# Optimization experiments

Hardware: AMD Instinct MI355X
Metric: run time of the kernel (lower is better)

The kernel has to match this reference:

```python
import jax, jax.numpy as jnp
import numpy as np

LEAKY_SLOPE = 0.2  # PyG GATConv default negative_slope
EPS = 1e-16


def _gat_layer(h_in, src, dst, W, a_src, a_dst, b, concat):
    # h_in: [N, Fin]; src/dst: [Etot] (self-loops included); W: [Fin, H*C]
    N = h_in.shape[0]
    H, C = a_src.shape
    h = (h_in @ W).reshape(N, H, C)                       # [N,H,C]
    al_s = jnp.sum(h * a_src, axis=-1)                    # [N,H]
    al_d = jnp.sum(h * a_dst, axis=-1)                    # [N,H]
    e = jax.nn.leaky_relu(al_s[src] + al_d[dst], LEAKY_SLOPE)  # [E,H]
    emax = jax.ops.segment_max(e, dst, num_segments=N)    # segment softmax over dst
    p = jnp.exp(e - emax[dst])
    denom = jax.ops.segment_sum(p, dst, num_segments=N)
    alpha = p / (denom[dst] + EPS)                        # [E,H]
    out = jax.ops.segment_sum(h[src] * alpha[:, :, None], dst, num_segments=N)  # [N,H,C]
    out = out.reshape(N, H * C) if concat else out.mean(axis=1)
    return out + b


def setup_inputs() -> dict:
    key = jax.random.key(0)
    ks = jax.random.split(key, 16)
    N, E, Fin, Hd, Hh = 10000, 320000, 256, 128, 4

    def glorot(k, shape, fan_in):
        return jax.random.normal(k, shape, dtype=jnp.float32) * (1.0 / np.sqrt(fan_in))

    inp = {
        "x": jax.random.normal(ks[0], (N, Fin), dtype=jnp.float32),
        "edge_index": jax.random.randint(ks[1], (2, E), 0, N, dtype=jnp.int32),
        # conv1: Fin -> Hd x Hh heads, concat
        "W1": glorot(ks[2], (Fin, Hh * Hd), Fin),
        "a1_src": glorot(ks[3], (Hh, Hd), Hd),
        "a1_dst": glorot(ks[4], (Hh, Hd), Hd),
        "b1": jnp.zeros((Hh * Hd,), jnp.float32),
        # conv2: Hh*Hd -> Hd x Hh heads, concat
        "W2": glorot(ks[5], (Hh * Hd, Hh * Hd), Hh * Hd),
        "a2_src": glorot(ks[6], (Hh, Hd), Hd),
        "a2_dst": glorot(ks[7], (Hh, Hd), Hd),
        "b2": jnp.zeros((Hh * Hd,), jnp.float32),
        # conv3: Hh*Hd -> Hd, 1 head, concat=False (mean)
        "W3": glorot(ks[8], (Hh * Hd, Hd), Hh * Hd),
        "a3_src": glorot(ks[9], (1, Hd), Hd),
        "a3_dst": glorot(ks[10], (1, Hd), Hd),
        "b3": jnp.zeros((Hd,), jnp.float32),
        # classifier: Hd -> Hd//2 -> 2
        "Wc1": glorot(ks[11], (Hd, Hd // 2), Hd),
        "bc1": jnp.zeros((Hd // 2,), jnp.float32),
        "Wc2": glorot(ks[12], (Hd // 2, 2), Hd // 2),
        "bc2": jnp.zeros((2,), jnp.float32),
    }
    return inp


def reference(x, edge_index, W1, a1_src, a1_dst, b1, W2, a2_src, a2_dst, b2,
              W3, a3_src, a3_dst, b3, Wc1, bc1, Wc2, bc2):
    N = x.shape[0]
    loops = jnp.arange(N, dtype=edge_index.dtype)
    src = jnp.concatenate([edge_index[0], loops])  # PyG adds self-loops
    dst = jnp.concatenate([edge_index[1], loops])

    h = jax.nn.elu(_gat_layer(x, src, dst, W1, a1_src, a1_dst, b1, concat=True))
    h = jax.nn.elu(_gat_layer(h, src, dst, W2, a2_src, a2_dst, b2, concat=True))
    embeddings = _gat_layer(h, src, dst, W3, a3_src, a3_dst, b3, concat=False)  # [N, 128]
    out = jax.nn.relu(embeddings @ Wc1 + bc1) @ Wc2 + bc2  # [N, 2]
    return out, embeddings
```

## Files before the change

kernel.cpp:

```cpp
#include <hip/hip_runtime.h>
#include <cstddef>

#define LEAKY 0.2f
#define EPS_DEN 1e-16f

typedef short bf8_t __attribute__((ext_vector_type(8)));
typedef float f4_t __attribute__((ext_vector_type(4)));
typedef unsigned short us4_t __attribute__((ext_vector_type(4)));

__device__ __forceinline__ unsigned short f2bf(float f) {
    unsigned u = __float_as_uint(f);
    unsigned r = (u + 0x7fffu + ((u >> 16) & 1u)) >> 16;
    return (unsigned short)r;
}
__device__ __forceinline__ float bf2f(unsigned short h) {
    return __uint_as_float(((unsigned)h) << 16);
}

__global__ void hist_kernel(const int* __restrict__ dst, int* __restrict__ counts, int E) {
    int i = blockIdx.x * blockDim.x + threadIdx.x;
    if (i < E) atomicAdd(&counts[dst[i]], 1);
}

__global__ void scan1_kernel(int* __restrict__ cnt, int* __restrict__ bsum, int N) {
    __shared__ int s[256];
    int t = threadIdx.x;
    int i = blockIdx.x * 256 + t;
    int v = (i < N) ? cnt[i] : 0;
    s[t] = v;
    __syncthreads();
#pragma unroll
    for (int st = 1; st < 256; st <<= 1) {
        int add = (t >= st) ? s[t - st] : 0;
        __syncthreads();
        s[t] += add;
        __syncthreads();
    }
    if (i < N) cnt[i] = s[t] - v;
    if (t == 255) bsum[blockIdx.x] = s[255];
}

__global__ void scan3b_kernel(int* __restrict__ cnt, const int* __restrict__ bsum,
                              int* __restrict__ offs, int N, int NB) {
    __shared__ int sPre[64];
    __shared__ int sTot;
    int t = threadIdx.x;
    if (t < 64) {
        int v = (t < NB) ? bsum[t] : 0;
        int inc = v;
#pragma unroll
        for (int off = 1; off < 64; off <<= 1) {
            int u = __shfl_up(inc, off);
            if (t >= off) inc += u;
        }
        sPre[t] = inc - v;
        if (t == 63) sTot = inc;
    }
    __syncthreads();
    int i = blockIdx.x * 256 + t;
    if (i < N) {
        int o = cnt[i] + sPre[blockIdx.x];
        offs[i] = o;
        cnt[i] = o;
    }
    if (blockIdx.x == 0 && t == 0) offs[N] = sTot;
}

__global__ void scatter_kernel(const int* __restrict__ src, const int* __restrict__ dst,
                               int* __restrict__ cursor, int* __restrict__ csrc, int E) {
    int i = blockIdx.x * blockDim.x + threadIdx.x;
    if (i < E) {
        int d = dst[i];
        int pos = atomicAdd(&cursor[d], 1);
        csrc[pos] = src[i];
    }
}

__global__ void split_all_kernel(
    const float* __restrict__ x, unsigned short* __restrict__ xh, unsigned short* __restrict__ xl,
    int NBX,
    const float* __restrict__ W1, unsigned short* __restrict__ w1h, unsigned short* __restrict__ w1l,
    const float* __restrict__ W2, unsigned short* __restrict__ w2h, unsigned short* __restrict__ w2l,
    const float* __restrict__ W3, unsigned short* __restrict__ w3h, unsigned short* __restrict__ w3l) {
    int b = blockIdx.x, t = threadIdx.x;
    float v;
    unsigned short* ph;
    unsigned short* pl;
    int idx;
    if (b < NBX) {
        idx = b * 256 + t;
        v = x[idx];
        ph = xh; pl = xl;
    } else if (b < NBX + 512) {
        idx = (b - NBX) * 256 + t;
        int n = idx >> 8, k = idx & 255;
        v = W1[(size_t)k * 512 + n];
        ph = w1h; pl = w1l;
    } else if (b < NBX + 512 + 1024) {
        idx = (b - NBX - 512) * 256 + t;
        int n = idx >> 9, k = idx & 511;
        v = W2[(size_t)k * 512 + n];
        ph = w2h; pl = w2l;
    } else {
        idx = (b - NBX - 1536) * 256 + t;
        int n = idx >> 9, k = idx & 511;
        v = W3[(size_t)k * 128 + n];
        ph = w3h; pl = w3l;
    }
    unsigned short hv = f2bf(v);
    ph[idx] = hv;
    pl[idx] = f2bf(v - bf2f(hv));
}

__global__ __launch_bounds__(256) void mfma_gemm128_kernel(
    const unsigned short* __restrict__ Ahi, const unsigned short* __restrict__ Alo,
    const unsigned short* __restrict__ BThi, const unsigned short* __restrict__ BTlo,
    const float* __restrict__ a_src, const float* __restrict__ a_dst,
    float* __restrict__ C, float* __restrict__ als, float* __restrict__ ald,
    int M, int N, int K) {
    constexpr int BK = 32;
    __shared__ __align__(16) unsigned short sAh[128 * BK];
    __shared__ __align__(16) unsigned short sAl[128 * BK];
    __shared__ __align__(16) unsigned short sBh[128 * BK];
    __shared__ __align__(16) unsigned short sBl[128 * BK];
    __shared__ float sAls[128][2];
    __shared__ float sAld[128][2];
    int t = threadIdx.x;
    int w = t >> 6, lane = t & 63;
    int quad = lane >> 4, low = lane & 15;
    int m0 = blockIdx.y * 128, n0 = blockIdx.x * 128;
    int wm = (w & 1) * 64, wn = (w >> 1) * 64;

    f4_t acc[4][4];
#pragma unroll
    for (int i = 0; i < 4; i++)
#pragma unroll
        for (int j = 0; j < 4; j++) acc[i][j] = (f4_t){0.f, 0.f, 0.f, 0.f};

    int srow = lane >> 2;
    int schunk = lane & 3;

    for (int k0 = 0; k0 < K; k0 += BK) {
        __syncthreads();
#pragma unroll
        for (int inst = 0; inst < 2; inst++) {
            int r = w * 32 + inst * 16 + srow;
            int gm = m0 + r;
            if (gm >= M) gm = M - 1;
            size_t goff = (size_t)gm * K + k0 + schunk * 8;
            size_t loff = (size_t)(w * 2048 + inst * 1024);
            __builtin_amdgcn_global_load_lds(
                (const __attribute__((address_space(1))) void*)(Ahi + goff),
                (__attribute__((address_space(3))) void*)((char*)sAh + loff), 16, 0, 0);
            __builtin_amdgcn_global_load_lds(
                (const __attribute__((address_space(1))) void*)(Alo + goff),
                (__attribute__((address_space(3))) void*)((char*)sAl + loff), 16, 0, 0);
        }
#pragma unroll
        for (int inst = 0; inst < 2; inst++) {
            int r = w * 32 + inst * 16 + srow;
            int gn = n0 + r;
            size_t goff = (size_t)gn * K + k0 + schunk * 8;
            size_t loff = (size_t)(w * 2048 + inst * 1024);
            __builtin_amdgcn_global_load_lds(
                (const __attribute__((address_space(1))) void*)(BThi + goff),
                (__attribute__((address_space(3))) void*)((char*)sBh + loff), 16, 0, 0);
            __builtin_amdgcn_global_load_lds(
                (const __attribute__((address_space(1))) void*)(BTlo + goff),
                (__attribute__((address_space(3))) void*)((char*)sBl + loff), 16, 0, 0);
        }
        __syncthreads();

        bf8_t afh[4], bfh[4], xx[4];
#pragma unroll
        for (int i = 0; i < 4; i++) {
            int row = wm + i * 16 + low;
            afh[i] = *(const bf8_t*)&sAh[row * BK + quad * 8];
        }
#pragma unroll
        for (int j = 0; j < 4; j++) {
            int row = wn + j * 16 + low;
            bfh[j] = *(const bf8_t*)&sBh[row * BK + quad * 8];
        }
#pragma unroll
        for (int i = 0; i < 4; i++)
#pragma unroll
            for (int j = 0; j < 4; j++)
                acc[i][j] = __builtin_amdgcn_mfma_f32_16x16x32_bf16(afh[i], bfh[j], acc[i][j], 0, 0, 0);
#pragma unroll
        for (int j = 0; j < 4; j++) {
            int row = wn + j * 16 + low;
            xx[j] = *(const bf8_t*)&sBl[row * BK + quad * 8];
        }
#pragma unroll
        for (int i = 0; i < 4; i++)
#pragma unroll
            for (int j = 0; j < 4; j++)
                acc[i][j] = __builtin_amdgcn_mfma_f32_16x16x32_bf16(afh[i], xx[j], acc[i][j], 0, 0, 0);
#pragma unroll
        for (int i = 0; i < 4; i++) {
            int row = wm + i * 16 + low;
            xx[i] = *(const bf8_t*)&sAl[row * BK + quad * 8];
        }
#pragma unroll
        for (int i = 0; i < 4; i++)
#pragma unroll
            for (int j = 0; j < 4; j++)
                acc[i][j] = __builtin_amdgcn_mfma_f32_16x16x32_bf16(xx[i], bfh[j], acc[i][j], 0, 0, 0);
    }

#pragma unroll
    for (int i = 0; i < 4; i++) {
#pragma unroll
        for (int r = 0; r < 4; r++) {
            int gm = m0 + wm + i * 16 + quad * 4 + r;
            if (gm >= M) continue;
#pragma unroll
            for (int j = 0; j < 4; j++) {
                int gn = n0 + wn + j * 16 + low;
                C[(size_t)gm * N + gn] = acc[i][j][r];
            }
        }
    }

    int hd = n0 >> 7;
    float as_[4], ad_[4];
#pragma unroll
    for (int j = 0; j < 4; j++) {
        int c = wn + j * 16 + low;
        as_[j] = a_src[hd * 128 + c];
        ad_[j] = a_dst[hd * 128 + c];
    }
    int chh = wn >> 6;
#pragma unroll
    for (int i = 0; i < 4; i++) {
#pragma unroll
        for (int r = 0; r < 4; r++) {
            float v = acc[i][0][r] * as_[0] + acc[i][1][r] * as_[1] +
                      acc[i][2][r] * as_[2] + acc[i][3][r] * as_[3];
            float vd = acc[i][0][r] * ad_[0] + acc[i][1][r] * ad_[1] +
                       acc[i][2][r] * ad_[2] + acc[i][3][r] * ad_[3];
#pragma unroll
            for (int off = 1; off < 16; off <<= 1) {
                v += __shfl_xor(v, off);
                vd += __shfl_xor(vd, off);
            }
            if (low == 0) {
                int row = wm + i * 16 + quad * 4 + r;
                sAls[row][chh] = v;
                sAld[row][chh] = vd;
            }
        }
    }
    __syncthreads();
    if (t < 128) {
        int gm = m0 + t;
        if (gm < M) {
            als[gm * 4 + hd] = sAls[t][0] + sAls[t][1];
            ald[gm * 4 + hd] = sAld[t][0] + sAld[t][1];
        }
    }
}

__global__ __launch_bounds__(256) void mfma_gemm64_kernel(
    const unsigned short* __restrict__ Ahi, const unsigned short* __restrict__ Alo,
    const unsigned short* __restrict__ BThi, const unsigned short* __restrict__ BTlo,
    const float* __restrict__ a_src, const float* __restrict__ a_dst,
    float* __restrict__ C, float* __restrict__ als, float* __restrict__ ald,
    int M, int N, int K) {
    constexpr int BK = 32;
    __shared__ __align__(16) unsigned short sAh[64 * BK];
    __shared__ __align__(16) unsigned short sAl[64 * BK];
    __shared__ __align__(16) unsigned short sBh[128 * BK];
    __shared__ __align__(16) unsigned short sBl[128 * BK];
    __shared__ float sAls[64][2];
    __shared__ float sAld[64][2];
    int t = threadIdx.x;
    int w = t >> 6, lane = t & 63;
    int quad = lane >> 4, low = lane & 15;
    int m0 = blockIdx.y * 64, n0 = blockIdx.x * 128;
    int wm = (w & 1) * 32, wn = (w >> 1) * 64;

    f4_t acc[2][4];
#pragma unroll
    for (int i = 0; i < 2; i++)
#pragma unroll
        for (int j = 0; j < 4; j++) acc[i][j] = (f4_t){0.f, 0.f, 0.f, 0.f};

    int srow = lane >> 2;
    int schunk = lane & 3;

    for (int k0 = 0; k0 < K; k0 += BK) {
        __syncthreads();
        {
            int gm = m0 + w * 16 + srow;
            if (gm >= M) gm = M - 1;
            size_t goff = (size_t)gm * K + k0 + schunk * 8;
            size_t loff = (size_t)(w * 1024);
            __builtin_amdgcn_global_load_lds(
                (const __attribute__((address_space(1))) void*)(Ahi + goff),
                (__attribute__((address_space(3))) void*)((char*)sAh + loff), 16, 0, 0);
            __builtin_amdgcn_global_load_lds(
                (const __attribute__((address_space(1))) void*)(Alo + goff),
                (__attribute__((address_space(3))) void*)((char*)sAl + loff), 16, 0, 0);
        }
#pragma unroll
        for (int inst = 0; inst < 2; inst++) {
            int gn = n0 + w * 32 + inst * 16 + srow;
            size_t goff = (size_t)gn * K + k0 + schunk * 8;
            size_t loff = (size_t)(w * 2048 + inst * 1024);
            __builtin_amdgcn_global_load_lds(
                (const __attribute__((address_space(1))) void*)(BThi + goff),
                (__attribute__((address_space(3))) void*)((char*)sBh + loff), 16, 0, 0);
            __builtin_amdgcn_global_load_lds(
                (const __attribute__((address_space(1))) void*)(BTlo + goff),
                (__attribute__((address_space(3))) void*)((char*)sBl + loff), 16, 0, 0);
        }
        __syncthreads();

        bf8_t afh[2], bfh[4], xx[4];
#pragma unroll
        for (int i = 0; i < 2; i++) {
            int row = wm + i * 16 + low;
            afh[i] = *(const bf8_t*)&sAh[row * BK + quad * 8];
        }
#pragma unroll
        for (int j = 0; j < 4; j++) {
            int row = wn + j * 16 + low;
            bfh[j] = *(const bf8_t*)&sBh[row * BK + quad * 8];
        }
#pragma unroll
        for (int i = 0; i < 2; i++)
#pragma unroll
            for (int j = 0; j < 4; j++)
                acc[i][j] = __builtin_amdgcn_mfma_f32_16x16x32_bf16(afh[i], bfh[j], acc[i][j], 0, 0, 0);
#pragma unroll
        for (int j = 0; j < 4; j++) {
            int row = wn + j * 16 + low;
            xx[j] = *(const bf8_t*)&sBl[row * BK + quad * 8];
        }
#pragma unroll
        for (int i = 0; i < 2; i++)
#pragma unroll
            for (int j = 0; j < 4; j++)
                acc[i][j] = __builtin_amdgcn_mfma_f32_16x16x32_bf16(afh[i], xx[j], acc[i][j], 0, 0, 0);
#pragma unroll
        for (int i = 0; i < 2; i++) {
            int row = wm + i * 16 + low;
            xx[i] = *(const bf8_t*)&sAl[row * BK + quad * 8];
        }
#pragma unroll
        for (int i = 0; i < 2; i++)
#pragma unroll
            for (int j = 0; j < 4; j++)
                acc[i][j] = __builtin_amdgcn_mfma_f32_16x16x32_bf16(xx[i], bfh[j], acc[i][j], 0, 0, 0);
    }

#pragma unroll
    for (int i = 0; i < 2; i++) {
#pragma unroll
        for (int r = 0; r < 4; r++) {
            int gm = m0 + wm + i * 16 + quad * 4 + r;
            if (gm >= M) continue;
#pragma unroll
            for (int j = 0; j < 4; j++) {
                int gn = n0 + wn + j * 16 + low;
                C[(size_t)gm * N + gn] = acc[i][j][r];
            }
        }
    }

    float as_[4], ad_[4];
#pragma unroll
    for (int j = 0; j < 4; j++) {
        int c = wn + j * 16 + low;
        as_[j] = a_src[c];
        ad_[j] = a_dst[c];
    }
    int chh = wn >> 6;
#pragma unroll
    for (int i = 0; i < 2; i++) {
#pragma unroll
        for (int r = 0; r < 4; r++) {
            float v = acc[i][0][r] * as_[0] + acc[i][1][r] * as_[1] +
                      acc[i][2][r] * as_[2] + acc[i][3][r] * as_[3];
            float vd = acc[i][0][r] * ad_[0] + acc[i][1][r] * ad_[1] +
                       acc[i][2][r] * ad_[2] + acc[i][3][r] * ad_[3];
#pragma unroll
            for (int off = 1; off < 16; off <<= 1) {
                v += __shfl_xor(v, off);
                vd += __shfl_xor(vd, off);
            }
            if (low == 0) {
                int row = wm + i * 16 + quad * 4 + r;
                sAls[row][chh] = v;
                sAld[row][chh] = vd;
            }
        }
    }
    __syncthreads();
    if (t < 64) {
        int gm = m0 + t;
        if (gm < M) {
            als[gm] = sAls[t][0] + sAls[t][1];
            ald[gm] = sAld[t][0] + sAld[t][1];
        }
    }
}

__global__ void stats_h4_kernel(const int* __restrict__ csrc, const int* __restrict__ offs,
                                const float* __restrict__ als, const float* __restrict__ ald,
                                float* __restrict__ pbuf, float* __restrict__ psf,
                                float* __restrict__ rden, int N, int E) {
    int wave = threadIdx.x >> 6, lane = threadIdx.x & 63;
    int n = blockIdx.x * 4 + wave;
    if (n >= N) return;
    int hd = lane & 3, es = lane >> 2;
    float aldn = ald[n * 4 + hd];
    float selfe = als[n * 4 + hd] + aldn;
    selfe = selfe > 0.f ? selfe : LEAKY * selfe;
    int beg = offs[n], end = offs[n + 1];
    int deg = end - beg;
    float* pb = pbuf + (size_t)hd * E;
    float m = selfe;
    float d = 0.f;
    if (deg <= 64) {
        float eR[4];
        int nch = (deg + 15) >> 4;
        for (int k = 0; k < nch; k++) {
            int idx = beg + k * 16 + es;
            float e = -1e30f;
            if (idx < end) {
                int s = csrc[idx];
                e = als[s * 4 + hd] + aldn;
                e = e > 0.f ? e : LEAKY * e;
                m = fmaxf(m, e);
            }
            eR[k] = e;
        }
#pragma unroll
        for (int off = 4; off < 64; off <<= 1) m = fmaxf(m, __shfl_xor(m, off));
        for (int k = 0; k < nch; k++) {
            int idx = beg + k * 16 + es;
            if (idx < end) {
                float p = __expf(eR[k] - m);
                pb[idx] = p;
                d += p;
            }
        }
    } else {
        for (int base = beg; base + es < end; base += 16) {
            int idx = base + es;
            int s = csrc[idx];
            float e = als[s * 4 + hd] + aldn;
            e = e > 0.f ? e : LEAKY * e;
            pb[idx] = e;
            m = fmaxf(m, e);
        }
#pragma unroll
        for (int off = 4; off < 64; off <<= 1) m = fmaxf(m, __shfl_xor(m, off));
        for (int base = beg; base + es < end; base += 16) {
            int idx = base + es;
            float p = __expf(pb[idx] - m);
            pb[idx] = p;
            d += p;
        }
    }
#pragma unroll
    for (int off = 4; off < 64; off <<= 1) d += __shfl_xor(d, off);
    float pself = __expf(selfe - m);
    float r = 1.0f / (d + pself + EPS_DEN);
    if (es == 0) {
        psf[n * 4 + hd] = pself;
        rden[n * 4 + hd] = r;
    }
}

template <bool DO_ELU>
__global__ __launch_bounds__(64) void gat_agg_hh_kernel(
    const float* __restrict__ h, const float* __restrict__ pbuf,
    const float* __restrict__ psf, const float* __restrict__ rden,
    const int* __restrict__ csrc, const int* __restrict__ offs,
    const float* __restrict__ bias, unsigned short* __restrict__ ohi,
    unsigned short* __restrict__ olo, int N, int E) {
    int gid = blockIdx.x;
    int hh = gid & 7;
    int n = gid >> 3;
    int head = hh >> 1;
    int lane = threadIdx.x;
    int eg = lane >> 4;
    int f0 = hh * 64 + (lane & 15) * 4;
    const float* pb = pbuf + (size_t)head * E;

    __shared__ int   sSrc[2][64];
    __shared__ float sP[2][64];
    int beg = offs[n], end = offs[n + 1];
    int nchunks = (end - beg + 63) >> 6;

    f4_t acc = (f4_t){0.f, 0.f, 0.f, 0.f};
    if (beg + lane < end) {
        sSrc[0][lane] = csrc[beg + lane] << 9;
        sP[0][lane] = pb[beg + lane];
    }
    for (int ch = 0; ch < nchunks; ch++) {
        int base = beg + ch * 64;
        int len = min(64, end - base);
        int buf = ch & 1;
        __syncthreads();
        int nbase = base + 64;
        if (ch + 1 < nchunks && nbase + lane < end) {
            sSrc[buf ^ 1][lane] = csrc[nbase + lane] << 9;
            sP[buf ^ 1][lane] = pb[nbase + lane];
        }
#pragma unroll 8
        for (int c = eg; c < len; c += 4) {
            const float* srow = h + (size_t)(unsigned)sSrc[buf][c] + f0;
            acc += sP[buf][c] * *(const f4_t*)srow;
        }
    }
    if (eg == 0) {
        f4_t x = *(const f4_t*)(h + (size_t)n * 512 + f0);
        acc += psf[n * 4 + head] * x;
    }
#pragma unroll
    for (int j = 0; j < 4; j++) {
        acc[j] += __shfl_xor(acc[j], 16);
        acc[j] += __shfl_xor(acc[j], 32);
    }
    if (lane < 16) {
        float r = rden[n * 4 + head];
        f4_t b = *(const f4_t*)(bias + f0);
        us4_t hs, ls;
#pragma unroll
        for (int j = 0; j < 4; j++) {
            float o = acc[j] * r + b[j];
            if (DO_ELU) o = o > 0.f ? o : (__expf(o) - 1.0f);
            unsigned short hv = f2bf(o);
            hs[j] = hv;
            ls[j] = f2bf(o - bf2f(hv));
        }
        size_t idx = (size_t)n * 512 + f0;
        *(us4_t*)&ohi[idx] = hs;
        *(us4_t*)&olo[idx] = ls;
    }
}

__global__ __launch_bounds__(64) void gat_agg_h1_cls_kernel(
    const float* __restrict__ h, const float* __restrict__ als,
    const float* __restrict__ ald, const int* __restrict__ csrc,
    const int* __restrict__ offs, const float* __restrict__ bias,
    const float* __restrict__ Wc1, const float* __restrict__ bc1,
    const float* __restrict__ Wc2, const float* __restrict__ bc2,
    float* __restrict__ emb, float* __restrict__ outp, int N) {
    int n = blockIdx.x;
    int lane = threadIdx.x;
    int eg = lane >> 4;
    int fl = (lane & 15) * 8;
    __shared__ int   sSrc[64];
    __shared__ float sP[64];
    __shared__ float semb[128];
    int beg = offs[n], end = offs[n + 1];
    int deg = end - beg;

    float aldn = ald[n];
    float selfe = als[n] + aldn;
    selfe = selfe > 0.f ? selfe : LEAKY * selfe;

    f4_t a0 = (f4_t){0.f, 0.f, 0.f, 0.f};
    f4_t a1 = (f4_t){0.f, 0.f, 0.f, 0.f};
    float d = 0.f;
    float m;

    if (deg <= 64) {
        float e = -1e30f;
        int s = 0;
        if (lane < deg) {
            s = csrc[beg + lane];
            e = als[s] + aldn;
            e = e > 0.f ? e : LEAKY * e;
        }
        m = fmaxf(e, selfe);
#pragma unroll
        for (int off = 1; off < 64; off <<= 1) m = fmaxf(m, __shfl_xor(m, off));
        float p = (lane < deg) ? __expf(e - m) : 0.f;
        d = p;
        sSrc[lane] = s << 7;
        sP[lane] = p;
        __syncthreads();
#pragma unroll 8
        for (int c = eg; c < deg; c += 4) {
            const float* srow = h + (size_t)(unsigned)sSrc[c] + fl;
            float pc = sP[c];
            a0 += pc * *(const f4_t*)(srow);
            a1 += pc * *(const f4_t*)(srow + 4);
        }
    } else {
        m = selfe;
        for (int i = beg + lane; i < end; i += 64) {
            int s = csrc[i];
            float e = als[s] + aldn;
            e = e > 0.f ? e : LEAKY * e;
            m = fmaxf(m, e);
        }
#pragma unroll
        for (int off = 1; off < 64; off <<= 1) m = fmaxf(m, __shfl_xor(m, off));
        for (int base = beg; base < end; base += 64) {
            int len = min(64, end - base);
            __syncthreads();
            if (lane < len) {
                int s = csrc[base + lane];
                float e = als[s] + aldn;
                e = e > 0.f ? e : LEAKY * e;
                float p = __expf(e - m);
                sSrc[lane] = s << 7;
                sP[lane] = p;
                d += p;
            }
            __syncthreads();
#pragma unroll 8
            for (int c = eg; c < len; c += 4) {
                const float* srow = h + (size_t)(unsigned)sSrc[c] + fl;
                float pc = sP[c];
                a0 += pc * *(const f4_t*)(srow);
                a1 += pc * *(const f4_t*)(srow + 4);
            }
        }
    }

    float pself = __expf(selfe - m);
    if (eg == 0) {
        const float* srow = h + (size_t)n * 128 + fl;
        a0 += pself * *(const f4_t*)(srow);
        a1 += pself * *(const f4_t*)(srow + 4);
    }
#pragma unroll
    for (int j = 0; j < 4; j++) {
        a0[j] += __shfl_xor(a0[j], 16);
        a0[j] += __shfl_xor(a0[j], 32);
        a1[j] += __shfl_xor(a1[j], 16);
        a1[j] += __shfl_xor(a1[j], 32);
    }
#pragma unroll
    for (int off = 1; off < 64; off <<= 1) d += __shfl_xor(d, off);
    float r = 1.0f / (d + pself + EPS_DEN);

    __syncthreads();
    if (lane < 16) {
        int fo = lane * 8;
        f4_t b0 = *(const f4_t*)(bias + fo);
        f4_t b1 = *(const f4_t*)(bias + fo + 4);
        f4_t o0, o1;
#pragma unroll
        for (int j = 0; j < 4; j++) {
            o0[j] = a0[j] * r + b0[j];
            o1[j] = a1[j] * r + b1[j];
        }
        *(f4_t*)&semb[fo] = o0;
        *(f4_t*)&semb[fo + 4] = o1;
        *(f4_t*)&emb[(size_t)n * 128 + fo] = o0;
        *(f4_t*)&emb[(size_t)n * 128 + fo + 4] = o1;
    }
    __syncthreads();

    float cacc = bc1[lane];
#pragma unroll 4
    for (int k = 0; k < 128; k++) cacc += semb[k] * Wc1[k * 64 + lane];
    cacc = fmaxf(cacc, 0.f);
    float o0 = cacc * Wc2[lane * 2 + 0];
    float o1 = cacc * Wc2[lane * 2 + 1];
#pragma unroll
    for (int off = 32; off; off >>= 1) {
        o0 += __shfl_down(o0, off);
        o1 += __shfl_down(o1, off);
    }
    if (lane == 0) {
        outp[n * 2 + 0] = o0 + bc2[0];
        outp[n * 2 + 1] = o1 + bc2[1];
    }
}

extern "C" void kernel_launch(void* const* d_in, const int* in_sizes, int n_in,
                              void* d_out, int out_size, void* d_ws, size_t ws_size,
                              hipStream_t stream) {
    const float* x      = (const float*)d_in[0];
    const int*   ei     = (const int*)d_in[1];
    const float* W1     = (const float*)d_in[2];
    const float* a1s    = (const float*)d_in[3];
    const float* a1d    = (const float*)d_in[4];
    const float* b1     = (const float*)d_in[5];
    const float* W2     = (const float*)d_in[6];
    const float* a2s    = (const float*)d_in[7];
    const float* a2d    = (const float*)d_in[8];
    const float* b2     = (const float*)d_in[9];
    const float* W3     = (const float*)d_in[10];
    const float* a3s    = (const float*)d_in[11];
    const float* a3d    = (const float*)d_in[12];
    const float* b3     = (const float*)d_in[13];
    const float* Wc1    = (const float*)d_in[14];
    const float* bc1    = (const float*)d_in[15];
    const float* Wc2    = (const float*)d_in[16];
    const float* bc2    = (const float*)d_in[17];

    const int N = in_sizes[0] / 256;
    const int E = in_sizes[1] / 2;
    const int F = 512;

    const int* src = ei;
    const int* dst = ei + E;

    auto align = [](size_t o) { return (o + 255) & ~(size_t)255; };
    size_t o = 0;
    size_t o_G     = o; o = align(o + (size_t)N * F * 4);
    size_t o_ahi   = o; o = align(o + (size_t)N * F * 2);
    size_t o_alo   = o; o = align(o + (size_t)N * F * 2);
    size_t o_xhi   = o; o = align(o + (size_t)N * 256 * 2);
    size_t o_xlo   = o; o = align(o + (size_t)N * 256 * 2);
    size_t o_w1h   = o; o = align(o + (size_t)512 * 256 * 2);
    size_t o_w1l   = o; o = align(o + (size_t)512 * 256 * 2);
    size_t o_w2h   = o; o = align(o + (size_t)512 * 512 * 2);
    size_t o_w2l   = o; o = align(o + (size_t)512 * 512 * 2);
    size_t o_w3h   = o; o = align(o + (size_t)128 * 512 * 2);
    size_t o_w3l   = o; o = align(o + (size_t)128 * 512 * 2);
    size_t o_als   = o; o = align(o + (size_t)N * 4 * 4);
    size_t o_ald   = o; o = align(o + (size_t)N * 4 * 4);
    size_t o_psf   = o; o = align(o + (size_t)N * 4 * 4);
    size_t o_rden  = o; o = align(o + (size_t)N * 4 * 4);
    size_t o_cnt   = o; o = align(o + (size_t)N * 4);
    size_t o_off   = o; o = align(o + (size_t)(N + 1) * 4);
    size_t o_bsum  = o; o = align(o + (size_t)64 * 4);
    size_t o_csrc  = o; o = align(o + (size_t)E * 4);
    size_t o_ebuf  = o; o = align(o + (size_t)E * 4 * 4);
    (void)ws_size;

    char* ws = (char*)d_ws;
    float* bufG  = (float*)(ws + o_G);
    unsigned short* act_hi = (unsigned short*)(ws + o_ahi);
    unsigned short* act_lo = (unsigned short*)(ws + o_alo);
    unsigned short* x_hi   = (unsigned short*)(ws + o_xhi);
    unsigned short* x_lo   = (unsigned short*)(ws + o_xlo);
    unsigned short* w1h = (unsigned short*)(ws + o_w1h);
    unsigned short* w1l = (unsigned short*)(ws + o_w1l);
    unsigned short* w2h = (unsigned short*)(ws + o_w2h);
    unsigned short* w2l = (unsigned short*)(ws + o_w2l);
    unsigned short* w3h = (unsigned short*)(ws + o_w3h);
    unsigned short* w3l = (unsigned short*)(ws + o_w3l);
    float* als  = (float*)(ws + o_als);
    float* ald  = (float*)(ws + o_ald);
    float* psf  = (float*)(ws + o_psf);
    float* rden = (float*)(ws + o_rden);
    int*   cnt  = (int*)(ws + o_cnt);
    int*   offs = (int*)(ws + o_off);
    int*   bsum = (int*)(ws + o_bsum);
    int*   csrc = (int*)(ws + o_csrc);
    float* ebuf = (float*)(ws + o_ebuf);

    float* outp = (float*)d_out;
    float* emb  = (float*)d_out + (size_t)N * 2;

    hipMemsetAsync(cnt, 0, (size_t)N * 4, stream);
    int eb = (E + 255) / 256;
    int nbs = (N + 255) / 256;
    hipLaunchKernelGGL(hist_kernel, dim3(eb), dim3(256), 0, stream, dst, cnt, E);
    hipLaunchKernelGGL(scan1_kernel, dim3(nbs), dim3(256), 0, stream, cnt, bsum, N);
    hipLaunchKernelGGL(scan3b_kernel, dim3(nbs), dim3(256), 0, stream, cnt, bsum, offs, N, nbs);
    hipLaunchKernelGGL(scatter_kernel, dim3(eb), dim3(256), 0, stream, src, dst, cnt, csrc, E);

    int NBX = N;
    hipLaunchKernelGGL(split_all_kernel, dim3(NBX + 512 + 1024 + 256), dim3(256), 0, stream,
                       x, x_hi, x_lo, NBX, W1, w1h, w1l, W2, w2h, w2l, W3, w3h, w3l);

    int nb4 = (N + 3) / 4;
    int gy128 = (N + 127) / 128;
    int gy64  = (N + 63) / 64;

    hipLaunchKernelGGL(mfma_gemm128_kernel, dim3(512 / 128, gy128), dim3(256), 0, stream,
                       x_hi, x_lo, w1h, w1l, a1s, a1d, bufG, als, ald, N, 512, 256);
    hipLaunchKernelGGL(stats_h4_kernel, dim3(nb4), dim3(256), 0, stream,
                       csrc, offs, als, ald, ebuf, psf, rden, N, E);
    hipLaunchKernelGGL((gat_agg_hh_kernel<true>), dim3(N * 8), dim3(64), 0, stream,
                       bufG, ebuf, psf, rden, csrc, offs, b1, act_hi, act_lo, N, E);

    hipLaunchKernelGGL(mfma_gemm128_kernel, dim3(512 / 128, gy128), dim3(256), 0, stream,
                       act_hi, act_lo, w2h, w2l, a2s, a2d, bufG, als, ald, N, 512, 512);
    hipLaunchKernelGGL(stats_h4_kernel, dim3(nb4), dim3(256), 0, stream,
                       csrc, offs, als, ald, ebuf, psf, rden, N, E);
    hipLaunchKernelGGL((gat_agg_hh_kernel<true>), dim3(N * 8), dim3(64), 0, stream,
                       bufG, ebuf, psf, rden, csrc, offs, b2, act_hi, act_lo, N, E);

    hipLaunchKernelGGL(mfma_gemm64_kernel, dim3(128 / 128, gy64), dim3(256), 0, stream,
                       act_hi, act_lo, w3h, w3l, a3s, a3d, bufG, als, ald, N, 128, 512);
    hipLaunchKernelGGL(gat_agg_h1_cls_kernel, dim3(N), dim3(64), 0, stream,
                       bufG, als, ald, csrc, offs, b3, Wc1, bc1, Wc2, bc2, emb, outp, N);
}
```

Baseline: 364.5 us.

## Double GEMM K-tile, pack four nodes per block in final aggregation

The bf16-split MFMA GEMM now stages a K-tile of 64 instead of 32, with wider row loads, and runs two 32-wide sub-steps per barrier pair. This halves the number of synchronisations and load phases, at the cost of twice the LDS per block and possibly lower occupancy. The last-layer aggregation and classifier kernel now handles four nodes per 256-thread block. It caches Wc1 in shared memory and passes edge source offsets and weights through wave shuffles instead of LDS plus barriers. The weight split kernel also reads W coalesced and scatters the transposed writes instead.

```diff
diff --git a/kernel.cpp b/kernel.cpp
--- a/kernel.cpp
+++ b/kernel.cpp
@@ -86,30 +86,34 @@
     float v;
     unsigned short* ph;
     unsigned short* pl;
-    int idx;
+    int out;
     if (b < NBX) {
-        idx = b * 256 + t;
+        int idx = b * 256 + t;
         v = x[idx];
+        out = idx;
         ph = xh; pl = xl;
     } else if (b < NBX + 512) {
-        idx = (b - NBX) * 256 + t;
-        int n = idx >> 8, k = idx & 255;
-        v = W1[(size_t)k * 512 + n];
+        int idx = (b - NBX) * 256 + t;
+        v = W1[idx];
+        int k = idx >> 9, n = idx & 511;
+        out = n * 256 + k;
         ph = w1h; pl = w1l;
     } else if (b < NBX + 512 + 1024) {
-        idx = (b - NBX - 512) * 256 + t;
-        int n = idx >> 9, k = idx & 511;
-        v = W2[(size_t)k * 512 + n];
+        int idx = (b - NBX - 512) * 256 + t;
+        v = W2[idx];
+        int k = idx >> 9, n = idx & 511;
+        out = n * 512 + k;
         ph = w2h; pl = w2l;
     } else {
-        idx = (b - NBX - 1536) * 256 + t;
-        int n = idx >> 9, k = idx & 511;
-        v = W3[(size_t)k * 128 + n];
+        int idx = (b - NBX - 1536) * 256 + t;
+        v = W3[idx];
+        int k = idx >> 7, n = idx & 127;
+        out = n * 512 + k;
         ph = w3h; pl = w3l;
     }
     unsigned short hv = f2bf(v);
-    ph[idx] = hv;
-    pl[idx] = f2bf(v - bf2f(hv));
+    ph[out] = hv;
+    pl[out] = f2bf(v - bf2f(hv));
 }
 
 __global__ __launch_bounds__(256) void mfma_gemm128_kernel(
@@ -118,7 +122,7 @@
     const float* __restrict__ a_src, const float* __restrict__ a_dst,
     float* __restrict__ C, float* __restrict__ als, float* __restrict__ ald,
     int M, int N, int K) {
-    constexpr int BK = 32;
+    constexpr int BK = 64;
     __shared__ __align__(16) unsigned short sAh[128 * BK];
     __shared__ __align__(16) unsigned short sAl[128 * BK];
     __shared__ __align__(16) unsigned short sBh[128 * BK];
@@ -137,18 +141,19 @@
 #pragma unroll
         for (int j = 0; j < 4; j++) acc[i][j] = (f4_t){0.f, 0.f, 0.f, 0.f};
 
-    int srow = lane >> 2;
-    int schunk = lane & 3;
+    int srow = lane >> 3;
+    int schunk = lane & 7;
 
     for (int k0 = 0; k0 < K; k0 += BK) {
         __syncthreads();
 #pragma unroll
-        for (int inst = 0; inst < 2; inst++) {
-            int r = w * 32 + inst * 16 + srow;
-            int gm = m0 + r;
+        for (int inst = 0; inst < 4; inst++) {
+            int rl = w * 32 + inst * 8 + srow;
+            int gm = m0 + rl;
             if (gm >= M) gm = M - 1;
             size_t goff = (size_t)gm * K + k0 + schunk * 8;
-            size_t loff = (size_t)(w * 2048 + inst * 1024);
+            size_t loff = (size_t)rl * 128 - (size_t)(lane * 16) + (size_t)(srow * 128 + schunk * 16);
+            loff = (size_t)(w * 32 + inst * 8) * 128;
             __builtin_amdgcn_global_load_lds(
                 (const __attribute__((address_space(1))) void*)(Ahi + goff),
                 (__attribute__((address_space(3))) void*)((char*)sAh + loff), 16, 0, 0);
@@ -157,11 +162,11 @@
                 (__attribute__((address_space(3))) void*)((char*)sAl + loff), 16, 0, 0);
         }
 #pragma unroll
-        for (int inst = 0; inst < 2; inst++) {
-            int r = w * 32 + inst * 16 + srow;
-            int gn = n0 + r;
+        for (int inst = 0; inst < 4; inst++) {
+            int rl = w * 32 + inst * 8 + srow;
+            int gn = n0 + rl;
             size_t goff = (size_t)gn * K + k0 + schunk * 8;
-            size_t loff = (size_t)(w * 2048 + inst * 1024);
+            size_t loff = (size_t)(w * 32 + inst * 8) * 128;
             __builtin_amdgcn_global_load_lds(
                 (const __attribute__((address_space(1))) void*)(BThi + goff),
                 (__attribute__((address_space(3))) void*)((char*)sBh + loff), 16, 0, 0);
@@ -171,42 +176,46 @@
         }
         __syncthreads();
 
-        bf8_t afh[4], bfh[4], xx[4];
-#pragma unroll
-        for (int i = 0; i < 4; i++) {
-            int row = wm + i * 16 + low;
-            afh[i] = *(const bf8_t*)&sAh[row * BK + quad * 8];
-        }
-#pragma unroll
-        for (int j = 0; j < 4; j++) {
-            int row = wn + j * 16 + low;
-            bfh[j] = *(const bf8_t*)&sBh[row * BK + quad * 8];
-        }
-#pragma unroll
-        for (int i = 0; i < 4; i++)
-#pragma unroll
-            for (int j = 0; j < 4; j++)
-                acc[i][j] = __builtin_amdgcn_mfma_f32_16x16x32_bf16(afh[i], bfh[j], acc[i][j], 0, 0, 0);
-#pragma unroll
-        for (int j = 0; j < 4; j++) {
-            int row = wn + j * 16 + low;
-            xx[j] = *(const bf8_t*)&sBl[row * BK + quad * 8];
-        }
-#pragma unroll
-        for (int i = 0; i < 4; i++)
-#pragma unroll
-            for (int j = 0; j < 4; j++)
-                acc[i][j] = __builtin_amdgcn_mfma_f32_16x16x32_bf16(afh[i], xx[j], acc[i][j], 0, 0, 0);
-#pragma unroll
-        for (int i = 0; i < 4; i++) {
-            int row = wm + i * 16 + low;
-            xx[i] = *(const bf8_t*)&sAl[row * BK + quad * 8];
-        }
-#pragma unroll
-        for (int i = 0; i < 4; i++)
-#pragma unroll
-            for (int j = 0; j < 4; j++)
-                acc[i][j] = __builtin_amdgcn_mfma_f32_16x16x32_bf16(xx[i], bfh[j], acc[i][j], 0, 0, 0);
+#pragma unroll
+        for (int ks = 0; ks < 2; ks++) {
+            int ko = ks * 32 + quad * 8;
+            bf8_t afh[4], bfh[4], xx[4];
+#pragma unroll
+            for (int i = 0; i < 4; i++) {
+                int row = wm + i * 16 + low;
+                afh[i] = *(const bf8_t*)&sAh[row * BK + ko];
+            }
+#pragma unroll
+            for (int j = 0; j < 4; j++) {
+                int row = wn + j * 16 + low;
+                bfh[j] = *(const bf8_t*)&sBh[row * BK + ko];
+            }
+#pragma unroll
+            for (int i = 0; i < 4; i++)
+#pragma unroll
+                for (int j = 0; j < 4; j++)
+                    acc[i][j] = __builtin_amdgcn_mfma_f32_16x16x32_bf16(afh[i], bfh[j], acc[i][j], 0, 0, 0);
+#pragma unroll
+            for (int j = 0; j < 4; j++) {
+                int row = wn + j * 16 + low;
+                xx[j] = *(const bf8_t*)&sBl[row * BK + ko];
+            }
+#pragma unroll
+            for (int i = 0; i < 4; i++)
+#pragma unroll
+                for (int j = 0; j < 4; j++)
+                    acc[i][j] = __builtin_amdgcn_mfma_f32_16x16x32_bf16(afh[i], xx[j], acc[i][j], 0, 0, 0);
+#pragma unroll
+            for (int i = 0; i < 4; i++) {
+                int row = wm + i * 16 + low;
+                xx[i] = *(const bf8_t*)&sAl[row * BK + ko];
+            }
+#pragma unroll
+            for (int i = 0; i < 4; i++)
+#pragma unroll
+                for (int j = 0; j < 4; j++)
+                    acc[i][j] = __builtin_amdgcn_mfma_f32_16x16x32_bf16(xx[i], bfh[j], acc[i][j], 0, 0, 0);
+        }
     }
 
 #pragma unroll
@@ -545,23 +554,26 @@
     }
 }
 
-__global__ __launch_bounds__(64) void gat_agg_h1_cls_kernel(
+__global__ __launch_bounds__(256) void gat_agg_h1_cls_kernel(
     const float* __restrict__ h, const float* __restrict__ als,
     const float* __restrict__ ald, const int* __restrict__ csrc,
     const int* __restrict__ offs, const float* __restrict__ bias,
     const float* __restrict__ Wc1, const float* __restrict__ bc1,
     const float* __restrict__ Wc2, const float* __restrict__ bc2,
     float* __restrict__ emb, float* __restrict__ outp, int N) {
-    int n = blockIdx.x;
-    int lane = threadIdx.x;
+    int tid = threadIdx.x;
+    int wave = tid >> 6;
+    int n = blockIdx.x * 4 + wave;
+    int lane = tid & 63;
     int eg = lane >> 4;
     int fl = (lane & 15) * 8;
-    __shared__ int   sSrc[64];
-    __shared__ float sP[64];
-    __shared__ float semb[128];
+    __shared__ float sW[128 * 64];
+    __shared__ float semb[4][128];
+
+    for (int i = tid; i < 128 * 64; i += 256) sW[i] = Wc1[i];
+
     int beg = offs[n], end = offs[n + 1];
     int deg = end - beg;
-
     float aldn = ald[n];
     float selfe = als[n] + aldn;
     selfe = selfe > 0.f ? selfe : LEAKY * selfe;
@@ -584,13 +596,14 @@
         for (int off = 1; off < 64; off <<= 1) m = fmaxf(m, __shfl_xor(m, off));
         float p = (lane < deg) ? __expf(e - m) : 0.f;
         d = p;
-        sSrc[lane] = s << 7;
-        sP[lane] = p;
-        __syncthreads();
-#pragma unroll 8
-        for (int c = eg; c < deg; c += 4) {
-            const float* srow = h + (size_t)(unsigned)sSrc[c] + fl;
-            float pc = sP[c];
+        int sreg = s << 7;
+        int maxit = (deg + 3) >> 2;
+#pragma unroll 4
+        for (int i = 0; i < maxit; i++) {
+            int c = eg + i * 4;
+            int soff = __shfl(sreg, c);
+            float pc = __shfl(p, c);
+            const float* srow = h + (size_t)(unsigned)soff + fl;
             a0 += pc * *(const f4_t*)(srow);
             a1 += pc * *(const f4_t*)(srow + 4);
         }
@@ -606,21 +619,23 @@
         for (int off = 1; off < 64; off <<= 1) m = fmaxf(m, __shfl_xor(m, off));
         for (int base = beg; base < end; base += 64) {
             int len = min(64, end - base);
-            __syncthreads();
+            int sreg = 0;
+            float p = 0.f;
             if (lane < len) {
                 int s = csrc[base + lane];
                 float e = als[s] + aldn;
                 e = e > 0.f ? e : LEAKY * e;
-                float p = __expf(e - m);
-                sSrc[lane] = s << 7;
-                sP[lane] = p;
+                p = __expf(e - m);
+                sreg = s << 7;
                 d += p;
             }
-            __syncthreads();
-#pragma unroll 8
-            for (int c = eg; c < len; c += 4) {
-                const float* srow = h + (size_t)(unsigned)sSrc[c] + fl;
-                float pc = sP[c];
+            int maxit = (len + 3) >> 2;
+#pragma unroll 4
+            for (int i = 0; i < maxit; i++) {
+                int c = eg + i * 4;
+                int soff = __shfl(sreg, c);
+                float pc = __shfl(p, c);
+                const float* srow = h + (size_t)(unsigned)soff + fl;
                 a0 += pc * *(const f4_t*)(srow);
                 a1 += pc * *(const f4_t*)(srow + 4);
             }
@@ -644,7 +659,6 @@
     for (int off = 1; off < 64; off <<= 1) d += __shfl_xor(d, off);
     float r = 1.0f / (d + pself + EPS_DEN);
 
-    __syncthreads();
     if (lane < 16) {
         int fo = lane * 8;
         f4_t b0 = *(const f4_t*)(bias + fo);
@@ -655,16 +669,16 @@
             o0[j] = a0[j] * r + b0[j];
             o1[j] = a1[j] * r + b1[j];
         }
-        *(f4_t*)&semb[fo] = o0;
-        *(f4_t*)&semb[fo + 4] = o1;
+        *(f4_t*)&semb[wave][fo] = o0;
+        *(f4_t*)&semb[wave][fo + 4] = o1;
         *(f4_t*)&emb[(size_t)n * 128 + fo] = o0;
         *(f4_t*)&emb[(size_t)n * 128 + fo + 4] = o1;
     }
     __syncthreads();
 
     float cacc = bc1[lane];
-#pragma unroll 4
-    for (int k = 0; k < 128; k++) cacc += semb[k] * Wc1[k * 64 + lane];
+#pragma unroll 8
+    for (int k = 0; k < 128; k++) cacc += semb[wave][k] * sW[k * 64 + lane];
     cacc = fmaxf(cacc, 0.f);
     float o0 = cacc * Wc2[lane * 2 + 0];
     float o1 = cacc * Wc2[lane * 2 + 1];
@@ -789,6 +803,6 @@
 
     hipLaunchKernelGGL(mfma_gemm64_kernel, dim3(128 / 128, gy64), dim3(256), 0, stream,
                        act_hi, act_lo, w3h, w3l, a3s, a3d, bufG, als, ald, N, 128, 512);
-    hipLaunchKernelGGL(gat_agg_h1_cls_kernel, dim3(N), dim3(64), 0, stream,
+    hipLaunchKernelGGL(gat_agg_h1_cls_kernel, dim3(nb4), dim3(256), 0, stream,
                        bufG, als, ald, csrc, offs, b3, Wc1, bc1, Wc2, bc2, emb, outp, N);
 }
```

Measured after the change: 355.8 us. 1.02x faster.
